# Performance work log

Hardware: AMD Instinct MI355X
Metric: run time of the kernel (lower is better)

## Reference

```python
import jax, jax.numpy as jnp
import numpy as np
from jax import lax

# db3 analysis filters (pywt convention)
DEC_LO = jnp.array([0.035226291882100656, -0.08544127388224149, -0.13501102001039084,
                    0.4598775021193313, 0.8068915093133388, 0.3326705529509569], jnp.float32)
DEC_HI = jnp.array([-0.3326705529509569, 0.8068915093133388, -0.4598775021193313,
                    -0.13501102001039084, 0.08544127388224149, 0.035226291882100656], jnp.float32)
REC_LO = DEC_LO[::-1]
REC_HI = DEC_HI[::-1]
DN = ('NCHW', 'OIHW', 'NCHW')


def _axis_conv(x, k, axis, stride=1, pad=0, dil=1):
    """Depthwise 1D correlation along axis 2 (H) or 3 (W) of an NCHW tensor."""
    C = x.shape[1]
    L = k.shape[0]
    if axis == 2:
        w = jnp.tile(k.reshape(1, 1, L, 1), (C, 1, 1, 1))
        strides, padding, ld = (stride, 1), ((pad, pad), (0, 0)), (dil, 1)
    else:
        w = jnp.tile(k.reshape(1, 1, 1, L), (C, 1, 1, 1))
        strides, padding, ld = (1, stride), ((0, 0), (pad, pad)), (1, dil)
    return lax.conv_general_dilated(x, w, strides, padding, lhs_dilation=ld,
                                    dimension_numbers=DN, feature_group_count=C)


def dwt2(x):
    """Single-level db3 DWT, zero padding (pytorch_wavelets AFB2D: rows then cols).
    Analysis correlation kernels are the reversed dec filters (= rec filters)."""
    lo_w = _axis_conv(x, REC_LO, 3, stride=2, pad=4)
    hi_w = _axis_conv(x, REC_HI, 3, stride=2, pad=4)
    ll = _axis_conv(lo_w, REC_LO, 2, stride=2, pad=4)
    lh = _axis_conv(lo_w, REC_HI, 2, stride=2, pad=4)
    hl = _axis_conv(hi_w, REC_LO, 2, stride=2, pad=4)
    hh = _axis_conv(hi_w, REC_HI, 2, stride=2, pad=4)
    return ll, lh, hl, hh


def idwt2(ll, lh, hl, hh):
    """Inverse db3 DWT (zero mode): zero-upsample (lhs_dilation=2) + correlate with
    flipped rec filters (= dec filters), pad = L-1-(L-2) = 1. Output = 2n-4."""
    lo_w = _axis_conv(ll, DEC_LO, 2, pad=1, dil=2) + _axis_conv(lh, DEC_HI, 2, pad=1, dil=2)
    hi_w = _axis_conv(hl, DEC_LO, 2, pad=1, dil=2) + _axis_conv(hh, DEC_HI, 2, pad=1, dil=2)
    return _axis_conv(lo_w, DEC_LO, 3, pad=1, dil=2) + _axis_conv(hi_w, DEC_HI, 3, pad=1, dil=2)


def dw3(x, w):
    """Depthwise 3x3 conv, padding 1, no bias. w: (C,1,3,3)."""
    return lax.conv_general_dilated(x, w, (1, 1), ((1, 1), (1, 1)),
                                    dimension_numbers=DN, feature_group_count=x.shape[1])


def conv1x1(x, w):
    return jnp.einsum('oc,bchw->bohw', w, x)


def l2norm(x):
    n = jnp.sqrt(jnp.sum(x * x, axis=-1, keepdims=True))
    return x / jnp.maximum(n, 1e-12)


def mfe(x, w1, w5, w7, w9):
    ll, lh, hl, hh = dwt2(x)
    return idwt2(dw3(ll, w1), dw3(lh, w5), dw3(hl, w7), dw3(hh, w9))


def setup_inputs() -> dict:
    B, C, H, W = 4, 64, 256, 256
    heads = 8
    key = jax.random.key(0)
    ks = jax.random.split(key, 12)
    s1 = 1.0 / np.sqrt(C)       # 1x1 conv fan-in
    s3 = 1.0 / 3.0              # depthwise 3x3 fan-in = 9
    return {
        'rgb_feat': jax.random.normal(ks[0], (B, C, H, W), jnp.float32),
        'depth_feat': jax.random.normal(ks[1], (B, C, H, W), jnp.float32),
        'temperature': jnp.ones((1, heads, 1, 1), jnp.float32),
        'w_qkv_rgb': jax.random.normal(ks[2], (2 * C, C), jnp.float32) * s1,
        'w_qkv_depth': jax.random.normal(ks[3], (2 * C, C), jnp.float32) * s1,
        'w_qkv_conv': jax.random.normal(ks[4], (2 * C, 1, 3, 3), jnp.float32) * s3,
        'w_mfe1': jax.random.normal(ks[5], (C, 1, 3, 3), jnp.float32) * s3,
        'w_mfe5': jax.random.normal(ks[6], (C, 1, 3, 3), jnp.float32) * s3,
        'w_mfe7': jax.random.normal(ks[7], (C, 1, 3, 3), jnp.float32) * s3,
        'w_mfe9': jax.random.normal(ks[8], (C, 1, 3, 3), jnp.float32) * s3,
        'w_proj': jax.random.normal(ks[9], (C, C), jnp.float32) * s1,
    }


def reference(rgb_feat, depth_feat, temperature, w_qkv_rgb, w_qkv_depth, w_qkv_conv,
              w_mfe1, w_mfe5, w_mfe7, w_mfe9, w_proj):
    b, c, h, w = rgb_feat.shape
    heads = temperature.shape[1]
    ch = c // heads
    hw = h * w

    # query from wavelet multi-frequency branch
    q_rgb = mfe(rgb_feat, w_mfe1, w_mfe5, w_mfe7, w_mfe9)

    # self path (rgb): 1x1 -> shared depthwise 3x3 -> split k,v
    kv_r = dw3(conv1x1(rgb_feat, w_qkv_rgb), w_qkv_conv)
    k_r, v_r = jnp.split(kv_r, 2, axis=1)
    q1 = q_rgb.reshape(b, heads, ch, hw)
    k1 = k_r.reshape(b, heads, ch, hw)
    v1 = v_r.reshape(b, heads, ch, hw)
    attn1 = jax.nn.softmax(
        jnp.einsum('bhcn,bhdn->bhcd', l2norm(q1), l2norm(k1)) * temperature, axis=-1)
    out_self = jnp.einsum('bhcd,bhdn->bhcn', attn1, v1).reshape(b, c, h, w)

    # cross path (depth), same shared depthwise conv; q1 NOT normalized here (as in torch)
    kv_d = dw3(conv1x1(depth_feat, w_qkv_depth), w_qkv_conv)
    k_d, v_d = jnp.split(kv_d, 2, axis=1)
    k2 = k_d.reshape(b, heads, ch, hw)
    v2 = v_d.reshape(b, heads, ch, hw)
    attn2 = jax.nn.softmax(
        jnp.einsum('bhcn,bhdn->bhcd', q1, l2norm(k2)) * temperature, axis=-1)
    out_cross = jnp.einsum('bhcd,bhdn->bhcn', attn2, v2).reshape(b, c, h, w)

    return conv1x1(out_self * out_cross, w_proj)
```

## Files before the change

### kernel.cpp

```cpp
#include <hip/hip_runtime.h>
#include <math.h>

#define B_ 4
#define C_ 64
#define H_ 256
#define W_ 256
#define N_ 65536
#define SB 130
#define SBSQ (SB*SB)

#define RL_INIT {0.3326705529509569f, 0.8068915093133388f, 0.4598775021193313f, -0.13501102001039084f, -0.08544127388224149f, 0.035226291882100656f}
#define RH_INIT {0.035226291882100656f, 0.08544127388224149f, -0.13501102001039084f, -0.4598775021193313f, 0.8068915093133388f, -0.3326705529509569f}
#define DL_INIT {0.035226291882100656f, -0.08544127388224149f, -0.13501102001039084f, 0.4598775021193313f, 0.8068915093133388f, 0.3326705529509569f}
#define DH_INIT {-0.3326705529509569f, 0.8068915093133388f, -0.4598775021193313f, -0.13501102001039084f, 0.08544127388224149f, 0.035226291882100656f}

__global__ __launch_bounds__(256) void k_dwt_dw3(
    const float* __restrict__ x,
    const float* __restrict__ w1, const float* __restrict__ w5,
    const float* __restrict__ w7, const float* __restrict__ w9,
    float* __restrict__ dsub)
{
  const float RL[6] = RL_INIT, RH[6] = RH_INIT;
  const int tx = blockIdx.x;
  const int ty = blockIdx.y;
  const int bc = blockIdx.z;
  const int c  = bc & 63;
  const int hs0 = ty * 16, ws0 = tx * 16;
  const int xrow0 = 2*hs0 - 6;
  const int xcol0 = 2*ws0 - 6;

  __shared__ float xs[40][40];
  __shared__ float tlo[40][18];
  __shared__ float thi[40][18];
  __shared__ float sub[4][18][18];

  const float* xp = x + (size_t)bc * N_;
  for (int i = threadIdx.x; i < 1600; i += 256) {
    int r = i / 40, cc = i % 40;
    int gr = xrow0 + r, gc = xcol0 + cc;
    float v = 0.f;
    if ((unsigned)gr < H_ && (unsigned)gc < W_) v = xp[gr * W_ + gc];
    xs[r][cc] = v;
  }
  __syncthreads();
  for (int i = threadIdx.x; i < 720; i += 256) {
    int r = i / 18, wsl = i % 18;
    float lo = 0.f, hi = 0.f;
#pragma unroll
    for (int t = 0; t < 6; ++t) {
      float v = xs[r][2*wsl + t];
      lo += v * RL[t];
      hi += v * RH[t];
    }
    tlo[r][wsl] = lo; thi[r][wsl] = hi;
  }
  __syncthreads();
  for (int i = threadIdx.x; i < 324; i += 256) {
    int hsl = i / 18, wsl = i % 18;
    float ll = 0.f, lh = 0.f, hl = 0.f, hh = 0.f;
#pragma unroll
    for (int t = 0; t < 6; ++t) {
      float a = tlo[2*hsl + t][wsl];
      float b = thi[2*hsl + t][wsl];
      ll += a * RL[t]; lh += a * RH[t];
      hl += b * RL[t]; hh += b * RH[t];
    }
    sub[0][hsl][wsl] = ll; sub[1][hsl][wsl] = lh;
    sub[2][hsl][wsl] = hl; sub[3][hsl][wsl] = hh;
  }
  __syncthreads();
  const int hsl = (threadIdx.x >> 4) + 1, wsl = (threadIdx.x & 15) + 1;
  const int hs = hs0 + hsl - 1, ws = ws0 + wsl - 1;
  if (hs < SB && ws < SB) {
    const float* wsel[4] = {w1 + c*9, w5 + c*9, w7 + c*9, w9 + c*9};
#pragma unroll
    for (int s = 0; s < 4; ++s) {
      float acc = 0.f;
#pragma unroll
      for (int dy = 0; dy < 3; ++dy)
#pragma unroll
        for (int dx = 0; dx < 3; ++dx)
          acc += sub[s][hsl + dy - 1][wsl + dx - 1] * wsel[s][dy*3 + dx];
      dsub[((size_t)s * 256 + bc) * SBSQ + hs * SB + ws] = acc;
    }
  }
}

__global__ __launch_bounds__(256) void k_idwt(
    const float* __restrict__ dsub,
    float* __restrict__ q,
    float* __restrict__ nq)
{
  const float DL[6] = DL_INIT, DH[6] = DH_INIT;
  const int bx = blockIdx.x, by = blockIdx.y, bc = blockIdx.z;
  const int h0 = by * 32, w0 = bx * 32;
  const int j0h = h0 >> 1, j0w = w0 >> 1;

  __shared__ float ds[4][18][18];
  __shared__ float lo2[32][18];
  __shared__ float hi2[32][18];

  for (int i = threadIdx.x; i < 4*18*18; i += 256) {
    int s = i / 324, rem = i % 324, r = rem / 18, cc = rem % 18;
    ds[s][r][cc] = dsub[((size_t)s * 256 + bc) * SBSQ + (j0h + r) * SB + (j0w + cc)];
  }
  __syncthreads();
  for (int i = threadIdx.x; i < 32*18; i += 256) {
    int hl = i / 18, wsl = i % 18;
    float lo = 0.f, hi = 0.f;
#pragma unroll
    for (int t = 0; t < 6; ++t) {
      int num = hl + t - 1;
      if ((num & 1) == 0) {
        int jl = num >> 1;
        lo += ds[0][jl][wsl] * DL[t] + ds[1][jl][wsl] * DH[t];
        hi += ds[2][jl][wsl] * DL[t] + ds[3][jl][wsl] * DH[t];
      }
    }
    lo2[hl][wsl] = lo; hi2[hl][wsl] = hi;
  }
  __syncthreads();
  float nqacc = 0.f;
  for (int i = threadIdx.x; i < 1024; i += 256) {
    int hl = i >> 5, wl = i & 31;
    float v = 0.f;
#pragma unroll
    for (int t = 0; t < 6; ++t) {
      int num = wl + t - 1;
      if ((num & 1) == 0) {
        int jl = num >> 1;
        v += lo2[hl][jl] * DL[t] + hi2[hl][jl] * DH[t];
      }
    }
    q[(size_t)bc * N_ + (h0 + hl) * W_ + (w0 + wl)] = v;
    nqacc += v * v;
  }
#pragma unroll
  for (int off = 32; off > 0; off >>= 1) nqacc += __shfl_down(nqacc, off, 64);
  __shared__ float red4[4];
  if ((threadIdx.x & 63) == 0) red4[threadIdx.x >> 6] = nqacc;
  __syncthreads();
  if (threadIdx.x == 0)
    atomicAdd(&nq[bc], red4[0] + red4[1] + red4[2] + red4[3]);
}

__global__ __launch_bounds__(256) void k_conv1x1(
    const float* __restrict__ x,
    const float* __restrict__ wq,
    const int co_off,
    float* __restrict__ out)
{
  const int b = blockIdx.y;
  const int n0 = blockIdx.x * 128;
  __shared__ float Xs[64][128];
  __shared__ float Wt[64][68];

  for (int i = threadIdx.x; i < 2048; i += 256) {
    int ci = i >> 5, f = i & 31;
    *(float4*)&Xs[ci][f * 4] =
        *(const float4*)&x[((size_t)b * 64 + ci) * N_ + n0 + f * 4];
  }
  for (int i = threadIdx.x; i < 4096; i += 256) {
    int co = i >> 6, ci = i & 63;
    Wt[ci][co] = wq[(co_off + co) * 64 + ci];
  }
  __syncthreads();

  const int px_g = threadIdx.x & 15;
  const int co_g = threadIdx.x >> 4;
  const int p0 = px_g * 4;
  float acc[4][8] = {};
#pragma unroll 2
  for (int ci = 0; ci < 64; ++ci) {
    float4 x0 = *(const float4*)&Xs[ci][p0];
    float4 x1 = *(const float4*)&Xs[ci][64 + p0];
    float4 wv = *(const float4*)&Wt[ci][co_g * 4];
    const float wr[4] = {wv.x, wv.y, wv.z, wv.w};
    const float xr[8] = {x0.x, x0.y, x0.z, x0.w, x1.x, x1.y, x1.z, x1.w};
#pragma unroll
    for (int i = 0; i < 4; ++i)
#pragma unroll
      for (int j = 0; j < 8; ++j)
        acc[i][j] += wr[i] * xr[j];
  }
#pragma unroll
  for (int i = 0; i < 4; ++i) {
    float* op = &out[((size_t)b * 64 + co_g * 4 + i) * N_ + n0];
    *(float4*)&op[p0]      = make_float4(acc[i][0], acc[i][1], acc[i][2], acc[i][3]);
    *(float4*)&op[64 + p0] = make_float4(acc[i][4], acc[i][5], acc[i][6], acc[i][7]);
  }
}

__global__ __launch_bounds__(256) void k_kred(
    const float* __restrict__ kpre,
    const float* __restrict__ q,
    const float* __restrict__ wc,
    float* __restrict__ S,
    float* __restrict__ nk)
{
  const int b = blockIdx.z, hd = blockIdx.y, tile = blockIdx.x;
  const int h0 = (tile >> 3) * 32, w0 = (tile & 7) * 32;
  const int d = threadIdx.x >> 5, lane = threadIdx.x & 31;
  const int ck = hd * 8 + d;

  __shared__ float ks[8][34][36];

  for (int i = threadIdx.x; i < 9248; i += 256) {
    int ch = i / 1156, rem = i % 1156;
    int r = rem / 34, cc = rem % 34;
    int gh = h0 - 1 + r, gw = w0 - 1 + cc;
    float v = 0.f;
    if ((unsigned)gh < H_ && (unsigned)gw < W_)
      v = kpre[((size_t)b * 64 + hd * 8 + ch) * N_ + gh * W_ + gw];
    ks[ch][r][cc] = v;
  }
  __syncthreads();

  float wk[9];
#pragma unroll
  for (int i = 0; i < 9; ++i) wk[i] = wc[ck * 9 + i];
  const float* qp = q + ((size_t)b * 64 + hd * 8) * N_;

  float sacc[8] = {};
  float nkacc = 0.f;
  for (int r = 0; r < 32; ++r) {
    float kv = 0.f;
#pragma unroll
    for (int dy = 0; dy < 3; ++dy)
#pragma unroll
      for (int dx = 0; dx < 3; ++dx)
        kv += ks[d][r + dy][lane + dx] * wk[dy * 3 + dx];
    nkacc += kv * kv;
    const size_t npix = (size_t)(h0 + r) * W_ + w0 + lane;
#pragma unroll
    for (int cc = 0; cc < 8; ++cc)
      sacc[cc] += qp[(size_t)cc * N_ + npix] * kv;
  }
#pragma unroll
  for (int m = 16; m >= 1; m >>= 1) {
#pragma unroll
    for (int cc = 0; cc < 8; ++cc) sacc[cc] += __shfl_xor(sacc[cc], m, 64);
    nkacc += __shfl_xor(nkacc, m, 64);
  }
  if (lane == 0) {
#pragma unroll
    for (int cc = 0; cc < 8; ++cc)
      atomicAdd(&S[(((size_t)b * 8 + hd) * 8 + cc) * 8 + d], sacc[cc]);
    atomicAdd(&nk[((size_t)b * 8 + hd) * 8 + d], nkacc);
  }
}

__global__ __launch_bounds__(256) void k_dw3v(
    const float* __restrict__ vpre,
    const float* __restrict__ wc,
    float* __restrict__ v)
{
  const int tile = blockIdx.x, cv = blockIdx.y, b = blockIdx.z;
  const int h0 = (tile >> 3) * 32, w0 = (tile & 7) * 32;
  __shared__ float vs[34][36];

  const float* vp = vpre + ((size_t)b * 64 + cv) * N_;
  for (int i = threadIdx.x; i < 1156; i += 256) {
    int r = i / 34, cc = i % 34;
    int gh = h0 - 1 + r, gw = w0 - 1 + cc;
    float val = 0.f;
    if ((unsigned)gh < H_ && (unsigned)gw < W_) val = vp[gh * W_ + gw];
    vs[r][cc] = val;
  }
  __syncthreads();

  float wk[9];
#pragma unroll
  for (int i = 0; i < 9; ++i) wk[i] = wc[(64 + cv) * 9 + i];

  for (int i = threadIdx.x; i < 1024; i += 256) {
    int r = i >> 5, cc = i & 31;
    float acc = 0.f;
#pragma unroll
    for (int dy = 0; dy < 3; ++dy)
#pragma unroll
      for (int dx = 0; dx < 3; ++dx)
        acc += vs[r + dy][cc + dx] * wk[dy * 3 + dx];
    v[((size_t)b * 64 + cv) * N_ + (h0 + r) * W_ + w0 + cc] = acc;
  }
}

__global__ __launch_bounds__(256) void k_attn(
    const float* __restrict__ S1, const float* __restrict__ S2,
    const float* __restrict__ nq, const float* __restrict__ nk1,
    const float* __restrict__ nk2, const float* __restrict__ temp,
    float* __restrict__ A1, float* __restrict__ A2)
{
  const int t = threadIdx.x;
  const int b = t >> 6, h = (t >> 3) & 7, c = t & 7;
  const float tp = temp[h];
  const float qn = fmaxf(sqrtf(nq[t]), 1e-12f);
  const size_t rowoff = (((size_t)b * 8 + h) * 8 + c) * 8;
  const size_t noff = ((size_t)b * 8 + h) * 8;

  float l[8];
#pragma unroll
  for (int d = 0; d < 8; ++d)
    l[d] = S1[rowoff + d] / (qn * fmaxf(sqrtf(nk1[noff + d]), 1e-12f)) * tp;
  float m = l[0];
#pragma unroll
  for (int d = 1; d < 8; ++d) m = fmaxf(m, l[d]);
  float sum = 0.f;
#pragma unroll
  for (int d = 0; d < 8; ++d) { l[d] = expf(l[d] - m); sum += l[d]; }
#pragma unroll
  for (int d = 0; d < 8; ++d) A1[rowoff + d] = l[d] / sum;

#pragma unroll
  for (int d = 0; d < 8; ++d)
    l[d] = S2[rowoff + d] / fmaxf(sqrtf(nk2[noff + d]), 1e-12f) * tp;
  m = l[0];
#pragma unroll
  for (int d = 1; d < 8; ++d) m = fmaxf(m, l[d]);
  sum = 0.f;
#pragma unroll
  for (int d = 0; d < 8; ++d) { l[d] = expf(l[d] - m); sum += l[d]; }
#pragma unroll
  for (int d = 0; d < 8; ++d) A2[rowoff + d] = l[d] / sum;
}

__global__ __launch_bounds__(256) void k_out(
    const float* __restrict__ vr, const float* __restrict__ vd,
    const float* __restrict__ A1, const float* __restrict__ A2,
    const float* __restrict__ P,
    float* __restrict__ out)
{
  const int b = blockIdx.y;
  const int n0 = blockIdx.x * 64;
  __shared__ float us[64][64];
  __shared__ float Pl[64][68];
  __shared__ float a1s[512], a2s[512];

  for (int i = threadIdx.x; i < 4096; i += 256) {
    int co = i >> 6, cc = i & 63;
    Pl[cc][co] = P[co * 64 + cc];
  }
  for (int i = threadIdx.x; i < 512; i += 256) {
    a1s[i] = A1[b * 512 + i];
    a2s[i] = A2[b * 512 + i];
  }
  __syncthreads();

  {
    const int px = threadIdx.x & 63;
    const int g = threadIdx.x >> 6;
    const int ch0 = g * 16;
    float vrr[16], vdd[16];
#pragma unroll
    for (int j = 0; j < 16; ++j) {
      vrr[j] = vr[((size_t)b * 64 + ch0 + j) * N_ + n0 + px];
      vdd[j] = vd[((size_t)b * 64 + ch0 + j) * N_ + n0 + px];
    }
#pragma unroll
    for (int j = 0; j < 16; ++j) {
      const int c = ch0 + j;
      const int base = (j & 8);
      float s = 0.f, t2 = 0.f;
#pragma unroll
      for (int dd = 0; dd < 8; ++dd) {
        s  += a1s[c * 8 + dd] * vrr[base + dd];
        t2 += a2s[c * 8 + dd] * vdd[base + dd];
      }
      us[c][px] = s * t2;
    }
  }
  __syncthreads();

  const int px_g = threadIdx.x & 15;
  const int co_g = threadIdx.x >> 4;
  const int p0 = px_g * 4;
  float acc[4][4] = {};
#pragma unroll 2
  for (int cc = 0; cc < 64; ++cc) {
    float4 uv = *(const float4*)&us[cc][p0];
    float4 pv = *(const float4*)&Pl[cc][co_g * 4];
    const float pr[4] = {pv.x, pv.y, pv.z, pv.w};
    const float ur[4] = {uv.x, uv.y, uv.z, uv.w};
#pragma unroll
    for (int i = 0; i < 4; ++i)
#pragma unroll
      for (int j = 0; j < 4; ++j)
        acc[i][j] += pr[i] * ur[j];
  }
#pragma unroll
  for (int i = 0; i < 4; ++i)
    *(float4*)&out[((size_t)b * 64 + co_g * 4 + i) * N_ + n0 + p0] =
        make_float4(acc[i][0], acc[i][1], acc[i][2], acc[i][3]);
}

extern "C" void kernel_launch(void* const* d_in, const int* in_sizes, int n_in,
                              void* d_out, int out_size, void* d_ws, size_t ws_size,
                              hipStream_t stream) {
  (void)in_sizes; (void)n_in; (void)out_size;
  const float* rgb  = (const float*)d_in[0];
  const float* dep  = (const float*)d_in[1];
  const float* temp = (const float*)d_in[2];
  const float* wqr  = (const float*)d_in[3];
  const float* wqd  = (const float*)d_in[4];
  const float* wqc  = (const float*)d_in[5];
  const float* w1   = (const float*)d_in[6];
  const float* w5   = (const float*)d_in[7];
  const float* w7   = (const float*)d_in[8];
  const float* w9   = (const float*)d_in[9];
  const float* wp   = (const float*)d_in[10];
  float* out = (float*)d_out;

  const size_t WS_NEEDED = 203475968;
  if (ws_size < WS_NEEDED) return;

  char* ws = (char*)d_ws;
  float* q   = (float*)(ws + 0);
  float* v_d = q;
  float* v_r = (float*)(ws + 67108864);
  float* big = (float*)(ws + 134217728);
  char* redb = ws + 203440128;
  float* S1  = (float*)(redb);
  float* S2  = (float*)(redb + 8192);
  float* nq  = (float*)(redb + 16384);
  float* nk1 = (float*)(redb + 17408);
  float* nk2 = (float*)(redb + 18432);
  float* A1  = (float*)(redb + 19456);
  float* A2  = (float*)(redb + 27648);

  hipMemsetAsync(redb, 0, 19456, stream);

  k_dwt_dw3<<<dim3(9, 9, 256), 256, 0, stream>>>(rgb, w1, w5, w7, w9, big);
  k_idwt<<<dim3(8, 8, 256), 256, 0, stream>>>(big, q, nq);

  k_conv1x1<<<dim3(512, 4), 256, 0, stream>>>(rgb, wqr, 0, big);
  k_kred<<<dim3(64, 8, 4), 256, 0, stream>>>(big, q, wqc, S1, nk1);
  k_conv1x1<<<dim3(512, 4), 256, 0, stream>>>(rgb, wqr, 64, big);
  k_dw3v<<<dim3(64, 64, 4), 256, 0, stream>>>(big, wqc, v_r);

  k_conv1x1<<<dim3(512, 4), 256, 0, stream>>>(dep, wqd, 0, big);
  k_kred<<<dim3(64, 8, 4), 256, 0, stream>>>(big, q, wqc, S2, nk2);
  k_conv1x1<<<dim3(512, 4), 256, 0, stream>>>(dep, wqd, 64, big);
  k_dw3v<<<dim3(64, 64, 4), 256, 0, stream>>>(big, wqc, v_d);

  k_attn<<<1, 256, 0, stream>>>(S1, S2, nq, nk1, nk2, temp, A1, A2);
  k_out<<<dim3(1024, 4), 256, 0, stream>>>(v_r, v_d, A1, A2, wp, out);
}
```

Baseline: 848.4 us.

## Fuse DWT, subband depthwise conv and IDWT into one tiled kernel; fold softmax into output

Merges the forward DWT plus subband 3x3 convs and the inverse DWT into a single kernel working on 64x64 output tiles with halo recompute in shared memory. This removes the global round-trip of the four subband tensors and one kernel launch. The attention softmax kernel is also removed: each output block now recomputes the 8x8 softmax rows from the Gram sums and norms. The cost is halo recomputation, larger shared memory use that may lower occupancy, and redundant softmax work in every output block.

```diff
diff --git a/kernel.cpp b/kernel.cpp
--- a/kernel.cpp
+++ b/kernel.cpp
@@ -6,132 +6,129 @@
 #define H_ 256
 #define W_ 256
 #define N_ 65536
-#define SB 130
-#define SBSQ (SB*SB)
 
 #define RL_INIT {0.3326705529509569f, 0.8068915093133388f, 0.4598775021193313f, -0.13501102001039084f, -0.08544127388224149f, 0.035226291882100656f}
 #define RH_INIT {0.035226291882100656f, 0.08544127388224149f, -0.13501102001039084f, -0.4598775021193313f, 0.8068915093133388f, -0.3326705529509569f}
 #define DL_INIT {0.035226291882100656f, -0.08544127388224149f, -0.13501102001039084f, 0.4598775021193313f, 0.8068915093133388f, 0.3326705529509569f}
 #define DH_INIT {-0.3326705529509569f, 0.8068915093133388f, -0.4598775021193313f, -0.13501102001039084f, 0.08544127388224149f, 0.035226291882100656f}
 
-__global__ __launch_bounds__(256) void k_dwt_dw3(
+__global__ __launch_bounds__(256) void k_mfe(
     const float* __restrict__ x,
     const float* __restrict__ w1, const float* __restrict__ w5,
     const float* __restrict__ w7, const float* __restrict__ w9,
-    float* __restrict__ dsub)
+    float* __restrict__ q, float* __restrict__ nq)
 {
   const float RL[6] = RL_INIT, RH[6] = RH_INIT;
-  const int tx = blockIdx.x;
-  const int ty = blockIdx.y;
+  const float DL[6] = DL_INIT, DH[6] = DH_INIT;
   const int bc = blockIdx.z;
   const int c  = bc & 63;
-  const int hs0 = ty * 16, ws0 = tx * 16;
-  const int xrow0 = 2*hs0 - 6;
-  const int xcol0 = 2*ws0 - 6;
-
-  __shared__ float xs[40][40];
-  __shared__ float tlo[40][18];
-  __shared__ float thi[40][18];
-  __shared__ float sub[4][18][18];
-
-  const float* xp = x + (size_t)bc * N_;
-  for (int i = threadIdx.x; i < 1600; i += 256) {
-    int r = i / 40, cc = i % 40;
-    int gr = xrow0 + r, gc = xcol0 + cc;
-    float v = 0.f;
-    if ((unsigned)gr < H_ && (unsigned)gc < W_) v = xp[gr * W_ + gc];
-    xs[r][cc] = v;
-  }
-  __syncthreads();
-  for (int i = threadIdx.x; i < 720; i += 256) {
-    int r = i / 18, wsl = i % 18;
+  const int h0 = blockIdx.y * 64, w0 = blockIdx.x * 64;
+
+  __shared__ float A[6240];
+  __shared__ float Bm[5928];
+  float* xs  = A;
+  float* sub = A;
+  float* lo2 = A;
+  float* hi2 = A + 2304;
+  float* tlo = Bm;
+  float* thi = Bm + 2964;
+  float* dt  = Bm;
+
+  float wk[4][9];
+#pragma unroll
+  for (int i = 0; i < 9; ++i) {
+    wk[0][i] = w1[c * 9 + i]; wk[1][i] = w5[c * 9 + i];
+    wk[2][i] = w7[c * 9 + i]; wk[3][i] = w9[c * 9 + i];
+  }
+
+  {
+    const float* xp = x + (size_t)bc * N_;
+    const int xr0 = h0 - 8, xc0 = w0 - 8;
+    for (int i = threadIdx.x; i < 78 * 39; i += 256) {
+      int r = i / 39, c2 = i % 39;
+      int gr = xr0 + r, gc = xc0 + c2 * 2;
+      float2 v = make_float2(0.f, 0.f);
+      if ((unsigned)gr < H_ && (unsigned)gc < W_)
+        v = *(const float2*)&xp[gr * W_ + gc];
+      *(float2*)&xs[r * 80 + c2 * 2] = v;
+    }
+  }
+  __syncthreads();
+
+  for (int i = threadIdx.x; i < 78 * 37; i += 256) {
+    int r = i / 37, sw = i % 37;
+    const float* xr = &xs[r * 80 + 2 * sw];
     float lo = 0.f, hi = 0.f;
 #pragma unroll
     for (int t = 0; t < 6; ++t) {
-      float v = xs[r][2*wsl + t];
-      lo += v * RL[t];
-      hi += v * RH[t];
-    }
-    tlo[r][wsl] = lo; thi[r][wsl] = hi;
-  }
-  __syncthreads();
-  for (int i = threadIdx.x; i < 324; i += 256) {
-    int hsl = i / 18, wsl = i % 18;
+      float v = xr[t];
+      lo += v * RL[t]; hi += v * RH[t];
+    }
+    tlo[r * 38 + sw] = lo; thi[r * 38 + sw] = hi;
+  }
+  __syncthreads();
+
+  for (int i = threadIdx.x; i < 37 * 37; i += 256) {
+    int sj = i / 37, sw = i % 37;
+    int base = (2 * sj) * 38 + sw;
     float ll = 0.f, lh = 0.f, hl = 0.f, hh = 0.f;
 #pragma unroll
     for (int t = 0; t < 6; ++t) {
-      float a = tlo[2*hsl + t][wsl];
-      float b = thi[2*hsl + t][wsl];
+      float a = tlo[base + t * 38];
+      float b = thi[base + t * 38];
       ll += a * RL[t]; lh += a * RH[t];
       hl += b * RL[t]; hh += b * RH[t];
     }
-    sub[0][hsl][wsl] = ll; sub[1][hsl][wsl] = lh;
-    sub[2][hsl][wsl] = hl; sub[3][hsl][wsl] = hh;
-  }
-  __syncthreads();
-  const int hsl = (threadIdx.x >> 4) + 1, wsl = (threadIdx.x & 15) + 1;
-  const int hs = hs0 + hsl - 1, ws = ws0 + wsl - 1;
-  if (hs < SB && ws < SB) {
-    const float* wsel[4] = {w1 + c*9, w5 + c*9, w7 + c*9, w9 + c*9};
+    sub[0 * 1406 + sj * 38 + sw] = ll;
+    sub[1 * 1406 + sj * 38 + sw] = lh;
+    sub[2 * 1406 + sj * 38 + sw] = hl;
+    sub[3 * 1406 + sj * 38 + sw] = hh;
+  }
+  __syncthreads();
+
+  for (int i = threadIdx.x; i < 34 * 34; i += 256) {
+    int dr = i / 34 + 1, dc = i % 34 + 1;
 #pragma unroll
     for (int s = 0; s < 4; ++s) {
+      const float* sp = &sub[s * 1406 + dr * 38 + dc];
       float acc = 0.f;
 #pragma unroll
       for (int dy = 0; dy < 3; ++dy)
 #pragma unroll
         for (int dx = 0; dx < 3; ++dx)
-          acc += sub[s][hsl + dy - 1][wsl + dx - 1] * wsel[s][dy*3 + dx];
-      dsub[((size_t)s * 256 + bc) * SBSQ + hs * SB + ws] = acc;
-    }
-  }
-}
-
-__global__ __launch_bounds__(256) void k_idwt(
-    const float* __restrict__ dsub,
-    float* __restrict__ q,
-    float* __restrict__ nq)
-{
-  const float DL[6] = DL_INIT, DH[6] = DH_INIT;
-  const int bx = blockIdx.x, by = blockIdx.y, bc = blockIdx.z;
-  const int h0 = by * 32, w0 = bx * 32;
-  const int j0h = h0 >> 1, j0w = w0 >> 1;
-
-  __shared__ float ds[4][18][18];
-  __shared__ float lo2[32][18];
-  __shared__ float hi2[32][18];
-
-  for (int i = threadIdx.x; i < 4*18*18; i += 256) {
-    int s = i / 324, rem = i % 324, r = rem / 18, cc = rem % 18;
-    ds[s][r][cc] = dsub[((size_t)s * 256 + bc) * SBSQ + (j0h + r) * SB + (j0w + cc)];
-  }
-  __syncthreads();
-  for (int i = threadIdx.x; i < 32*18; i += 256) {
-    int hl = i / 18, wsl = i % 18;
+          acc += sp[dy * 38 + dx] * wk[s][dy * 3 + dx];
+      dt[s * 1260 + dr * 36 + dc] = acc;
+    }
+  }
+  __syncthreads();
+
+  for (int i = threadIdx.x; i < 64 * 34; i += 256) {
+    int hl = i / 34, dc = i % 34 + 1;
+    int idx0 = (hl >> 1) + 1;
+    int po = hl & 1;
     float lo = 0.f, hi = 0.f;
 #pragma unroll
-    for (int t = 0; t < 6; ++t) {
-      int num = hl + t - 1;
-      if ((num & 1) == 0) {
-        int jl = num >> 1;
-        lo += ds[0][jl][wsl] * DL[t] + ds[1][jl][wsl] * DH[t];
-        hi += ds[2][jl][wsl] * DL[t] + ds[3][jl][wsl] * DH[t];
-      }
-    }
-    lo2[hl][wsl] = lo; hi2[hl][wsl] = hi;
-  }
-  __syncthreads();
+    for (int o = 0; o < 3; ++o) {
+      int rr = (idx0 + o) * 36 + dc;
+      float cl = DL[2 * o + 1 - po], ch = DH[2 * o + 1 - po];
+      lo += dt[0 * 1260 + rr] * cl + dt[1 * 1260 + rr] * ch;
+      hi += dt[2 * 1260 + rr] * cl + dt[3 * 1260 + rr] * ch;
+    }
+    lo2[hl * 36 + dc] = lo; hi2[hl * 36 + dc] = hi;
+  }
+  __syncthreads();
+
   float nqacc = 0.f;
-  for (int i = threadIdx.x; i < 1024; i += 256) {
-    int hl = i >> 5, wl = i & 31;
+  for (int i = threadIdx.x; i < 4096; i += 256) {
+    int hl = i >> 6, wl = i & 63;
+    int ci0 = (wl >> 1) + 1;
+    int po = wl & 1;
+    const float* lr = &lo2[hl * 36 + ci0];
+    const float* hr = &hi2[hl * 36 + ci0];
     float v = 0.f;
 #pragma unroll
-    for (int t = 0; t < 6; ++t) {
-      int num = wl + t - 1;
-      if ((num & 1) == 0) {
-        int jl = num >> 1;
-        v += lo2[hl][jl] * DL[t] + hi2[hl][jl] * DH[t];
-      }
-    }
+    for (int o = 0; o < 3; ++o)
+      v += lr[o] * DL[2 * o + 1 - po] + hr[o] * DH[2 * o + 1 - po];
     q[(size_t)bc * N_ + (h0 + hl) * W_ + (w0 + wl)] = v;
     nqacc += v * v;
   }
@@ -285,48 +282,11 @@
   }
 }
 
-__global__ __launch_bounds__(256) void k_attn(
+__global__ __launch_bounds__(256) void k_out(
+    const float* __restrict__ vr, const float* __restrict__ vd,
     const float* __restrict__ S1, const float* __restrict__ S2,
     const float* __restrict__ nq, const float* __restrict__ nk1,
     const float* __restrict__ nk2, const float* __restrict__ temp,
-    float* __restrict__ A1, float* __restrict__ A2)
-{
-  const int t = threadIdx.x;
-  const int b = t >> 6, h = (t >> 3) & 7, c = t & 7;
-  const float tp = temp[h];
-  const float qn = fmaxf(sqrtf(nq[t]), 1e-12f);
-  const size_t rowoff = (((size_t)b * 8 + h) * 8 + c) * 8;
-  const size_t noff = ((size_t)b * 8 + h) * 8;
-
-  float l[8];
-#pragma unroll
-  for (int d = 0; d < 8; ++d)
-    l[d] = S1[rowoff + d] / (qn * fmaxf(sqrtf(nk1[noff + d]), 1e-12f)) * tp;
-  float m = l[0];
-#pragma unroll
-  for (int d = 1; d < 8; ++d) m = fmaxf(m, l[d]);
-  float sum = 0.f;
-#pragma unroll
-  for (int d = 0; d < 8; ++d) { l[d] = expf(l[d] - m); sum += l[d]; }
-#pragma unroll
-  for (int d = 0; d < 8; ++d) A1[rowoff + d] = l[d] / sum;
-
-#pragma unroll
-  for (int d = 0; d < 8; ++d)
-    l[d] = S2[rowoff + d] / fmaxf(sqrtf(nk2[noff + d]), 1e-12f) * tp;
-  m = l[0];
-#pragma unroll
-  for (int d = 1; d < 8; ++d) m = fmaxf(m, l[d]);
-  sum = 0.f;
-#pragma unroll
-  for (int d = 0; d < 8; ++d) { l[d] = expf(l[d] - m); sum += l[d]; }
-#pragma unroll
-  for (int d = 0; d < 8; ++d) A2[rowoff + d] = l[d] / sum;
-}
-
-__global__ __launch_bounds__(256) void k_out(
-    const float* __restrict__ vr, const float* __restrict__ vd,
-    const float* __restrict__ A1, const float* __restrict__ A2,
     const float* __restrict__ P,
     float* __restrict__ out)
 {
@@ -340,9 +300,36 @@
     int co = i >> 6, cc = i & 63;
     Pl[cc][co] = P[co * 64 + cc];
   }
-  for (int i = threadIdx.x; i < 512; i += 256) {
-    a1s[i] = A1[b * 512 + i];
-    a2s[i] = A2[b * 512 + i];
+  if (threadIdx.x < 64) {
+    const int t = threadIdx.x;
+    const int h = t >> 3;
+    const float tp = temp[h];
+    const float qn = fmaxf(sqrtf(nq[b * 64 + t]), 1e-12f);
+    const size_t rowoff = ((size_t)b * 64 + t) * 8;
+    const size_t noff = ((size_t)b * 8 + h) * 8;
+    float l[8];
+#pragma unroll
+    for (int d = 0; d < 8; ++d)
+      l[d] = S1[rowoff + d] / (qn * fmaxf(sqrtf(nk1[noff + d]), 1e-12f)) * tp;
+    float m = l[0];
+#pragma unroll
+    for (int d = 1; d < 8; ++d) m = fmaxf(m, l[d]);
+    float sum = 0.f;
+#pragma unroll
+    for (int d = 0; d < 8; ++d) { l[d] = expf(l[d] - m); sum += l[d]; }
+#pragma unroll
+    for (int d = 0; d < 8; ++d) a1s[t * 8 + d] = l[d] / sum;
+#pragma unroll
+    for (int d = 0; d < 8; ++d)
+      l[d] = S2[rowoff + d] / fmaxf(sqrtf(nk2[noff + d]), 1e-12f) * tp;
+    m = l[0];
+#pragma unroll
+    for (int d = 1; d < 8; ++d) m = fmaxf(m, l[d]);
+    sum = 0.f;
+#pragma unroll
+    for (int d = 0; d < 8; ++d) { l[d] = expf(l[d] - m); sum += l[d]; }
+#pragma unroll
+    for (int d = 0; d < 8; ++d) a2s[t * 8 + d] = l[d] / sum;
   }
   __syncthreads();
 
@@ -424,13 +411,10 @@
   float* nq  = (float*)(redb + 16384);
   float* nk1 = (float*)(redb + 17408);
   float* nk2 = (float*)(redb + 18432);
-  float* A1  = (float*)(redb + 19456);
-  float* A2  = (float*)(redb + 27648);
 
   hipMemsetAsync(redb, 0, 19456, stream);
 
-  k_dwt_dw3<<<dim3(9, 9, 256), 256, 0, stream>>>(rgb, w1, w5, w7, w9, big);
-  k_idwt<<<dim3(8, 8, 256), 256, 0, stream>>>(big, q, nq);
+  k_mfe<<<dim3(4, 4, 256), 256, 0, stream>>>(rgb, w1, w5, w7, w9, q, nq);
 
   k_conv1x1<<<dim3(512, 4), 256, 0, stream>>>(rgb, wqr, 0, big);
   k_kred<<<dim3(64, 8, 4), 256, 0, stream>>>(big, q, wqc, S1, nk1);
@@ -442,6 +426,6 @@
   k_conv1x1<<<dim3(512, 4), 256, 0, stream>>>(dep, wqd, 64, big);
   k_dw3v<<<dim3(64, 64, 4), 256, 0, stream>>>(big, wqc, v_d);
 
-  k_attn<<<1, 256, 0, stream>>>(S1, S2, nq, nk1, nk2, temp, A1, A2);
-  k_out<<<dim3(1024, 4), 256, 0, stream>>>(v_r, v_d, A1, A2, wp, out);
-}
+  k_out<<<dim3(1024, 4), 256, 0, stream>>>(v_r, v_d, S1, S2, nq, nk1, nk2,
+                                           temp, wp, out);
+}
```

Result: faster. 763.6 us (-10.0%).
